# Performance work log

Hardware: AMD Instinct MI355X
Metric: run time of the kernel (lower is better)

The kernel has to match this reference:

```python
import jax, jax.numpy as jnp
import numpy as np

EPS = 1e-5
FH, FW, OC = 1, 9, 32  # filt_h, filt_w, out_channels (hardcoded in HypER)


def _bn(x, g, b, axes):
    # training-mode batchnorm: biased variance over `axes`
    m = jnp.mean(x, axis=axes, keepdims=True)
    v = jnp.mean(jnp.square(x - m), axis=axes, keepdims=True)
    return (x - m) * jax.lax.rsqrt(v + EPS) * g + b


def setup_inputs() -> dict:
    key = jax.random.key(0)
    ks = jax.random.split(key, 8)
    N, INPUT_D, D1, D2, B = 50000, 400, 400, 400, 8192
    fc_len = OC * (D1 - FW + 1)  # 32*392 = 12544
    return {
        "head_tail_id": jax.random.randint(ks[0], (2, B), 0, N, dtype=jnp.int32),
        "unique_entity_embed": jax.random.normal(ks[1], (N, INPUT_D), jnp.float32),
        "W_E": jax.random.normal(ks[2], (INPUT_D, D1), jnp.float32) * 0.05,
        "fc1_w": jax.random.normal(ks[3], (OC * FW, D2), jnp.float32) * 0.05,
        "fc1_b": jnp.zeros((OC * FW,), jnp.float32),
        "fc_w": jax.random.normal(ks[4], (D1, fc_len), jnp.float32) * 0.02,
        "fc_b": jnp.zeros((D1,), jnp.float32),
        "bn0_g": jnp.ones((1,), jnp.float32),
        "bn0_b": jnp.zeros((1,), jnp.float32),
        "bn1_g": jnp.ones((OC,), jnp.float32),
        "bn1_b": jnp.zeros((OC,), jnp.float32),
        "bn2_g": jnp.ones((400,), jnp.float32),
        "bn2_b": jnp.zeros((400,), jnp.float32),
    }


def reference(head_tail_id, unique_entity_embed, W_E, fc1_w, fc1_b, fc_w, fc_b,
              bn0_g, bn0_b, bn1_g, bn1_b, bn2_g, bn2_b):
    E = unique_entity_embed @ W_E                    # (N, d1)
    head = E[head_tail_id[0]]                        # (B, d1)
    tail = E[head_tail_id[1]]                        # (B, d1)
    # bn0: BatchNorm2d with 1 channel -> normalize over all B*1*d1 elements
    x = _bn(head, bn0_g[0], bn0_b[0], axes=(0, 1))   # (B, d1)
    # hypernetwork: per-sample dynamic 1x9 filters for 32 out-channels
    k = (tail @ fc1_w.T + fc1_b).reshape(-1, OC, FW)  # (B, 32, 9)
    W_out = x.shape[1] - FW + 1                       # d1-8 = 392
    win_idx = jnp.arange(W_out)[:, None] + jnp.arange(FW)[None, :]
    xw = x[:, win_idx]                                # (B, W_out, 9) sliding windows
    # grouped conv (groups=B), cross-correlation as in F.conv2d
    conv = jnp.einsum('bjw,bow->boj', xw, k)          # (B, 32, W_out)
    # bn1: per out-channel over (B, W_out)
    conv = _bn(conv, bn1_g[None, :, None], bn1_b[None, :, None], axes=(0, 2))
    feat = conv.reshape(conv.shape[0], -1)            # (B, 32*W_out), channel-major flatten
    out = feat @ fc_w.T + fc_b                        # (B, d1)
    out = _bn(out, bn2_g, bn2_b, axes=(0,))           # BatchNorm1d over batch
    return jax.nn.relu(out)
```

## Files before the change

kernel.cpp:

```cpp
#include <hip/hip_runtime.h>


#define BB   8192
#define DD   400
#define RR   288
#define OCC  32
#define FWW  9
#define JJ   392
#define FCLEN 12544
#define KSPL 4
#define KS   (FCLEN / KSPL)
#define KSTEPS (KS / 64)
#define EPSF 1e-5
#define RB2  512

typedef __attribute__((ext_vector_type(8))) short bf16x8;
typedef __attribute__((ext_vector_type(4))) float f32x4;

__device__ inline unsigned short f2bf(float f) {
    union { float f; unsigned u; } x; x.f = f;
    unsigned r = x.u + 0x7fffu + ((x.u >> 16) & 1u);
    return (unsigned short)(r >> 16);
}

__device__ inline void gload16(const void* g, void* l) {
    __builtin_amdgcn_global_load_lds((const __attribute__((address_space(1))) unsigned int*)g,
                                     (__attribute__((address_space(3))) unsigned int*)l, 16, 0, 0);
}

__device__ inline float block_reduce_256(float v, float* red) {
    #pragma unroll
    for (int m = 1; m < 64; m <<= 1) v += __shfl_xor(v, m);
    int wv = threadIdx.x >> 6;
    if ((threadIdx.x & 63) == 0) red[wv] = v;
    __syncthreads();
    float r = 0.f;
    if (threadIdx.x == 0) r = red[0] + red[1] + red[2] + red[3];
    return r;
}

__global__ __launch_bounds__(256) void prep_M(const float* __restrict__ WE,
                                              const float* __restrict__ f1w,
                                              float* __restrict__ Mout) {
    __shared__ float sA[16][17];
    __shared__ float sB[16][17];
    int tx = threadIdx.x, ty = threadIdx.y;
    int r0 = blockIdx.x * 16, i0 = blockIdx.y * 16;
    float acc = 0.f;
    for (int d0 = 0; d0 < DD; d0 += 16) {
        sA[ty][tx] = WE[(size_t)(i0 + ty) * DD + d0 + tx];
        sB[ty][tx] = f1w[(size_t)(r0 + ty) * DD + d0 + tx];
        __syncthreads();
        #pragma unroll
        for (int dd = 0; dd < 16; ++dd) acc = fmaf(sA[ty][dd], sB[tx][dd], acc);
        __syncthreads();
    }
    Mout[(size_t)(i0 + ty) * RR + r0 + tx] = acc;
}

template <int BN>
__global__ __launch_bounds__(256) void gemm_s1(const float* __restrict__ A,
                                               const int* __restrict__ idx,
                                               const float* __restrict__ Bm,
                                               const float* __restrict__ bias,
                                               float* __restrict__ C, int N,
                                               float* __restrict__ bn0part) {
    constexpr int BNF = BN / 16;
    constexpr int BCH = 64 * (BN / 4) / 256;
    __shared__ unsigned short Al[64][72];
    __shared__ unsigned short Bl[BN][72];
    __shared__ int ridx[64];
    __shared__ float red[8];
    int tid = threadIdx.x;
    int bm = blockIdx.x, bn = blockIdx.y;
    if (tid < 64) ridx[tid] = idx[bm * 64 + tid];
    int lane = tid & 63, wv = tid >> 6;
    int m16 = lane & 15, kb = lane >> 4;
    f32x4 acc[BNF];
    #pragma unroll
    for (int nb = 0; nb < BNF; ++nb) acc[nb] = (f32x4){0.f, 0.f, 0.f, 0.f};
    __syncthreads();

    float4 av[4];
    float4 bv[BCH];
    auto LOADR = [&](int k0) {
        #pragma unroll
        for (int r = 0; r < 4; ++r) {
            int c = tid + 256 * r;
            int row = c >> 4, kq = c & 15;
            int gk = k0 + kq * 4;
            av[r] = (float4){0.f, 0.f, 0.f, 0.f};
            if (gk < DD) av[r] = *(const float4*)(A + (size_t)ridx[row] * DD + gk);
        }
        #pragma unroll
        for (int r = 0; r < BCH; ++r) {
            int c = tid + 256 * r;
            int kk2 = c / (BN / 4), nq = c % (BN / 4);
            int gk = k0 + kk2;
            bv[r] = (float4){0.f, 0.f, 0.f, 0.f};
            if (gk < DD) bv[r] = *(const float4*)(Bm + (size_t)gk * N + bn * BN + nq * 4);
        }
    };
    auto WRITELDS = [&]() {
        #pragma unroll
        for (int r = 0; r < 4; ++r) {
            int c = tid + 256 * r;
            int row = c >> 4, kq = c & 15;
            ushort4 p;
            p.x = f2bf(av[r].x); p.y = f2bf(av[r].y); p.z = f2bf(av[r].z); p.w = f2bf(av[r].w);
            *(ushort4*)&Al[row][kq * 4] = p;
        }
        #pragma unroll
        for (int r = 0; r < BCH; ++r) {
            int c = tid + 256 * r;
            int kk2 = c / (BN / 4), nq = c % (BN / 4);
            Bl[nq * 4 + 0][kk2] = f2bf(bv[r].x);
            Bl[nq * 4 + 1][kk2] = f2bf(bv[r].y);
            Bl[nq * 4 + 2][kk2] = f2bf(bv[r].z);
            Bl[nq * 4 + 3][kk2] = f2bf(bv[r].w);
        }
    };

    LOADR(0);
    for (int kt = 0; kt < 7; ++kt) {
        WRITELDS();
        __syncthreads();
        if (kt + 1 < 7) LOADR((kt + 1) * 64);
        #pragma unroll
        for (int ks = 0; ks < 2; ++ks) {
            bf16x8 a = *(const bf16x8*)&Al[wv * 16 + m16][ks * 32 + kb * 8];
            #pragma unroll
            for (int nb = 0; nb < BNF; ++nb) {
                bf16x8 b = *(const bf16x8*)&Bl[nb * 16 + m16][ks * 32 + kb * 8];
                acc[nb] = __builtin_amdgcn_mfma_f32_16x16x32_bf16(a, b, acc[nb], 0, 0, 0);
            }
        }
        __syncthreads();
    }
    float s1 = 0.f, s2 = 0.f;
    #pragma unroll
    for (int nb = 0; nb < BNF; ++nb)
        #pragma unroll
        for (int rr = 0; rr < 4; ++rr) {
            int gr = bm * 64 + wv * 16 + kb * 4 + rr;
            int gc = bn * BN + nb * 16 + m16;
            float v = acc[nb][rr];
            if (bias) v += bias[gc];
            C[(size_t)gr * N + gc] = v;
            s1 += v; s2 = fmaf(v, v, s2);
        }
    if (bn0part) {
        float t1 = block_reduce_256(s1, red);
        __syncthreads();
        float t2 = block_reduce_256(s2, red);
        if (tid == 0) {
            int pid = bm * gridDim.y + bn;
            bn0part[pid * 2] = t1; bn0part[pid * 2 + 1] = t2;
        }
    }
}

__global__ __launch_bounds__(256) void bn0_fin(const float* __restrict__ part,
                                               const float* __restrict__ g,
                                               const float* __restrict__ b,
                                               float* __restrict__ ab0) {
    __shared__ float red[8];
    float s1 = 0.f, s2 = 0.f;
    for (int i = threadIdx.x; i < 640; i += 256) {
        s1 += part[i * 2]; s2 += part[i * 2 + 1];
    }
    float t1 = block_reduce_256(s1, red);
    __syncthreads();
    float t2 = block_reduce_256(s2, red);
    if (threadIdx.x == 0) {
        double n = (double)BB * DD;
        double mean = (double)t1 / n;
        double var = (double)t2 / n - mean * mean;
        float a0 = (float)((double)g[0] / sqrt(var + EPSF));
        float b0 = (float)((double)b[0] - mean * a0);
        ab0[0] = a0; ab0[1] = b0;
    }
}

__global__ __launch_bounds__(256) void conv_k(const float* __restrict__ head,
                                              const float* __restrict__ kbuf,
                                              const float* __restrict__ ab0,
                                              unsigned short* __restrict__ convb,
                                              float* __restrict__ chpartT) {
    __shared__ float xs[DD];
    __shared__ float ks[RR];
    int b = blockIdx.x, tid = threadIdx.x;
    float a0 = ab0[0], b0 = ab0[1];
    for (int i = tid; i < DD; i += 256) xs[i] = fmaf(head[(size_t)b * DD + i], a0, b0);
    for (int i = tid; i < RR; i += 256) ks[i] = kbuf[(size_t)b * RR + i];
    __syncthreads();
    int lane = tid & 63, wv = tid >> 6;
    unsigned short* orow = convb + (size_t)b * FCLEN;
    float kk[8][FWW];
    #pragma unroll
    for (int oi = 0; oi < 8; ++oi)
        #pragma unroll
        for (int w2 = 0; w2 < FWW; ++w2) kk[oi][w2] = ks[(wv * 8 + oi) * FWW + w2];
    float s1[8], s2[8];
    #pragma unroll
    for (int oi = 0; oi < 8; ++oi) { s1[oi] = 0.f; s2[oi] = 0.f; }
    #pragma unroll
    for (int jt = 0; jt < 2; ++jt) {
        int j0 = jt * 256 + lane * 4;
        if (j0 < JJ) {
            const float4* x4 = (const float4*)xs;
            float4 va = x4[(j0 >> 2)], vb = x4[(j0 >> 2) + 1], vc = x4[(j0 >> 2) + 2];
            float x[12] = {va.x, va.y, va.z, va.w, vb.x, vb.y, vb.z, vb.w, vc.x, vc.y, vc.z, vc.w};
            #pragma unroll
            for (int oi = 0; oi < 8; ++oi) {
                float acc[4];
                #pragma unroll
                for (int q = 0; q < 4; ++q) {
                    float a = 0.f;
                    #pragma unroll
                    for (int w2 = 0; w2 < FWW; ++w2) a = fmaf(x[q + w2], kk[oi][w2], a);
                    acc[q] = a;
                }
                ushort4 p;
                p.x = f2bf(acc[0]); p.y = f2bf(acc[1]); p.z = f2bf(acc[2]); p.w = f2bf(acc[3]);
                *(ushort4*)(orow + (wv * 8 + oi) * JJ + j0) = p;
                #pragma unroll
                for (int q = 0; q < 4; ++q) { s1[oi] += acc[q]; s2[oi] = fmaf(acc[q], acc[q], s2[oi]); }
            }
        }
    }
    #pragma unroll
    for (int oi = 0; oi < 8; ++oi) {
        float a = s1[oi], c = s2[oi];
        #pragma unroll
        for (int m = 1; m < 64; m <<= 1) { a += __shfl_xor(a, m); c += __shfl_xor(c, m); }
        if (lane == 0) {
            int o = wv * 8 + oi;
            chpartT[(size_t)o * BB + b] = a;
            chpartT[(size_t)(OCC + o) * BB + b] = c;
        }
    }
}

__global__ __launch_bounds__(256) void bn1_fin(const float* __restrict__ chpartT,
                                               const float* __restrict__ g1,
                                               const float* __restrict__ b1,
                                               float* __restrict__ alphabeta) {
    __shared__ float red[8];
    int o = blockIdx.x, tid = threadIdx.x;
    float s1 = 0.f, s2 = 0.f;
    for (int t = tid; t < BB; t += 256) {
        s1 += chpartT[(size_t)o * BB + t];
        s2 += chpartT[(size_t)(OCC + o) * BB + t];
    }
    float t1 = block_reduce_256(s1, red);
    __syncthreads();
    float t2 = block_reduce_256(s2, red);
    if (tid == 0) {
        double n = (double)BB * JJ;
        double mean = (double)t1 / n;
        double var = (double)t2 / n - mean * mean;
        float al = (float)((double)g1[o] / sqrt(var + EPSF));
        float be = (float)((double)b1[o] - mean * al);
        alphabeta[o] = al; alphabeta[OCC + o] = be;
    }
}

__global__ __launch_bounds__(256) void prep_fcw(const float* __restrict__ fc_w,
                                                const float* __restrict__ fc_b,
                                                const float* __restrict__ alphabeta,
                                                unsigned short* __restrict__ Bp,
                                                float* __restrict__ bias2) {
    __shared__ float al[OCC], be[OCC];
    __shared__ float red[8];
    int d = blockIdx.x, tid = threadIdx.x;
    if (tid < OCC) { al[tid] = alphabeta[tid]; be[tid] = alphabeta[OCC + tid]; }
    __syncthreads();
    const float* row = fc_w + (size_t)d * FCLEN;
    unsigned short* orow = Bp + (size_t)d * FCLEN;
    float bacc = 0.f;
    for (int o = 0; o < OCC; ++o) {
        float a = al[o], bb = be[o];
        for (int j = tid; j < JJ; j += 256) {
            float wv = row[o * JJ + j];
            orow[o * JJ + j] = f2bf(wv * a);
            bacc = fmaf(wv, bb, bacc);
        }
    }
    float t = block_reduce_256(bacc, red);
    if (tid == 0) bias2[d] = fc_b[d] + t;
}

__global__ __launch_bounds__(256, 3) void fc_gemm_sk(const unsigned short* __restrict__ A,
                                                     const unsigned short* __restrict__ Bp,
                                                     float* __restrict__ P) {
    __shared__ __align__(16) unsigned short Al[256 * 64];
    __shared__ __align__(16) unsigned short Bl[80 * 64];
    int tid = threadIdx.x;
    int orig = blockIdx.x;
    int wgid = (orig & 7) * 80 + (orig >> 3);
    int bn = wgid % 5;
    int rest = wgid / 5;
    int bm = rest & 31;
    int bz = rest >> 5;
    int lane = tid & 63, wv = tid >> 6;
    int m16 = lane & 15, kb = lane >> 4;
    int srow = lane >> 3, scol = lane & 7;
    int sw = m16 & 7;
    f32x4 acc[4][5];
    #pragma unroll
    for (int mi = 0; mi < 4; ++mi)
        #pragma unroll
        for (int nb = 0; nb < 5; ++nb) acc[mi][nb] = (f32x4){0.f, 0.f, 0.f, 0.f};

    const unsigned short* Asrc = A + (size_t)(bm * 256 + srow) * FCLEN
                                   + (size_t)bz * KS + ((scol ^ srow) << 3);
    const unsigned short* Bsrc = Bp + (size_t)(bn * 80 + srow) * FCLEN
                                   + (size_t)bz * KS + ((scol ^ srow) << 3);

    for (int kt = 0; kt < KSTEPS; ++kt) {
        const size_t koff = (size_t)kt * 64;
        #pragma unroll
        for (int i = 0; i < 11; ++i) {
            int c = wv + i * 4;
            if (c < 32) {
                gload16(Asrc + (size_t)c * 8 * FCLEN + koff, Al + c * 512);
            } else if (c < 42) {
                int cb = c - 32;
                gload16(Bsrc + (size_t)cb * 8 * FCLEN + koff, Bl + cb * 512);
            }
        }
        __syncthreads();
        #pragma unroll
        for (int ks2 = 0; ks2 < 2; ++ks2) {
            int ch = (((ks2 * 4 + kb) ^ sw) << 3);
            bf16x8 a[4];
            #pragma unroll
            for (int mi = 0; mi < 4; ++mi)
                a[mi] = *(const bf16x8*)(Al + (wv * 64 + mi * 16 + m16) * 64 + ch);
            #pragma unroll
            for (int nb = 0; nb < 5; ++nb) {
                bf16x8 b = *(const bf16x8*)(Bl + (nb * 16 + m16) * 64 + ch);
                #pragma unroll
                for (int mi = 0; mi < 4; ++mi)
                    acc[mi][nb] = __builtin_amdgcn_mfma_f32_16x16x32_bf16(a[mi], b, acc[mi][nb], 0, 0, 0);
            }
        }
        __syncthreads();
    }

    float* Po = P + (size_t)bz * BB * DD;
    #pragma unroll
    for (int mi = 0; mi < 4; ++mi)
        #pragma unroll
        for (int nb = 0; nb < 5; ++nb)
            #pragma unroll
            for (int rr = 0; rr < 4; ++rr) {
                int gr = bm * 256 + wv * 64 + mi * 16 + kb * 4 + rr;
                int gc = bn * 80 + nb * 16 + m16;
                Po[(size_t)gr * DD + gc] = acc[mi][nb][rr];
            }
}

__global__ __launch_bounds__(256) void reduce_bn2(const float* __restrict__ P,
                                                  const float* __restrict__ bias2,
                                                  float* __restrict__ out,
                                                  float* __restrict__ part) {
    int blk = blockIdx.x, tid = threadIdx.x;
    int r0 = blk * 16;
    const size_t S = (size_t)BB * DD;
    bool hasb = tid < DD - 256;
    float bia = bias2[tid];
    float bib = hasb ? bias2[256 + tid] : 0.f;
    float s1a = 0.f, s2a = 0.f, s1b = 0.f, s2b = 0.f;
    for (int r = 0; r < 16; ++r) {
        size_t base = (size_t)(r0 + r) * DD;
        float v = P[base + tid] + P[S + base + tid] + P[2 * S + base + tid] + P[3 * S + base + tid] + bia;
        out[base + tid] = v;
        s1a += v; s2a = fmaf(v, v, s2a);
        if (hasb) {
            size_t b2i = base + 256 + tid;
            float u = P[b2i] + P[S + b2i] + P[2 * S + b2i] + P[3 * S + b2i] + bib;
            out[b2i] = u;
            s1b += u; s2b = fmaf(u, u, s2b);
        }
    }
    float* p = part + (size_t)blk * (DD * 2);
    p[tid * 2] = s1a; p[tid * 2 + 1] = s2a;
    if (hasb) { p[(256 + tid) * 2] = s1b; p[(256 + tid) * 2 + 1] = s2b; }
}

__global__ __launch_bounds__(128) void bn2_fin(const float* __restrict__ part,
                                               const float* __restrict__ g2,
                                               const float* __restrict__ b2,
                                               float* __restrict__ sc,
                                               float* __restrict__ sh) {
    __shared__ float red[4];
    int col = blockIdx.x, tid = threadIdx.x;
    float s1 = 0.f, s2 = 0.f;
    for (int t = tid; t < RB2; t += 128) {
        s1 += part[(size_t)t * (DD * 2) + col * 2];
        s2 += part[(size_t)t * (DD * 2) + col * 2 + 1];
    }
    #pragma unroll
    for (int m = 1; m < 64; m <<= 1) { s1 += __shfl_xor(s1, m); s2 += __shfl_xor(s2, m); }
    int wv = tid >> 6;
    if ((tid & 63) == 0) { red[wv] = s1; red[2 + wv] = s2; }
    __syncthreads();
    if (tid == 0) {
        double t1 = (double)red[0] + red[1];
        double t2 = (double)red[2] + red[3];
        double mean = t1 / (double)BB;
        double var = t2 / (double)BB - mean * mean;
        float s = (float)((double)g2[col] / sqrt(var + EPSF));
        sc[col] = s;
        sh[col] = (float)((double)b2[col] - mean * s);
    }
}

__global__ __launch_bounds__(256) void final_k(float* __restrict__ out,
                                               const float* __restrict__ sc,
                                               const float* __restrict__ sh) {
    __shared__ float lsc[DD], lsh[DD];
    int tid = threadIdx.x;
    for (int c = tid; c < DD; c += 256) { lsc[c] = sc[c]; lsh[c] = sh[c]; }
    __syncthreads();
    size_t base = (size_t)blockIdx.x * 4 * DD;
    for (int r = 0; r < 4; ++r)
        for (int c = tid; c < DD; c += 256) {
            size_t i = base + (size_t)r * DD + c;
            float v = fmaf(out[i], lsc[c], lsh[c]);
            out[i] = v > 0.f ? v : 0.f;
        }
}

extern "C" void kernel_launch(void* const* d_in, const int* in_sizes, int n_in,
                              void* d_out, int out_size, void* d_ws, size_t ws_size,
                              hipStream_t stream) {
    const int* ht      = (const int*)d_in[0];
    const float* UE    = (const float*)d_in[1];
    const float* W_E   = (const float*)d_in[2];
    const float* fc1_w = (const float*)d_in[3];
    const float* fc1_b = (const float*)d_in[4];
    const float* fc_w  = (const float*)d_in[5];
    const float* fc_b  = (const float*)d_in[6];
    const float* bn0_g = (const float*)d_in[7];
    const float* bn0_b = (const float*)d_in[8];
    const float* bn1_g = (const float*)d_in[9];
    const float* bn1_b = (const float*)d_in[10];
    const float* bn2_g = (const float*)d_in[11];
    const float* bn2_b = (const float*)d_in[12];
    float* out = (float*)d_out;

    char* w = (char*)d_ws;
    unsigned short* convb = (unsigned short*)w; w += (size_t)BB * FCLEN * 2;
    unsigned short* Bprep = (unsigned short*)w; w += (size_t)DD * FCLEN * 2;
    float* chpartT = (float*)w; w += (size_t)2 * OCC * BB * 4;
    float* bn0p = (float*)w;  w += 640 * 2 * 4;
    float* ab0 = (float*)w;   w += 64;
    float* alphabeta = (float*)w; w += 64 * 4;
    float* bias2 = (float*)w; w += DD * 4;
    float* bn2p = (float*)w;  w += (size_t)RB2 * DD * 2 * 4;
    float* bn2sc = (float*)w; w += DD * 4;
    float* bn2sh = (float*)w; w += DD * 4;
    float* P = (float*)w;     w += (size_t)KSPL * BB * DD * 4;
    float* head = P;
    float* kbuf = head + (size_t)BB * DD;
    float* Mbuf = kbuf + (size_t)BB * RR;
    (void)ws_size; (void)in_sizes; (void)n_in; (void)out_size;

    prep_M<<<dim3(RR / 16, DD / 16), dim3(16, 16), 0, stream>>>(W_E, fc1_w, Mbuf);
    gemm_s1<80><<<dim3(BB / 64, DD / 80), 256, 0, stream>>>(UE, ht, W_E, nullptr, head, DD, bn0p);
    gemm_s1<96><<<dim3(BB / 64, RR / 96), 256, 0, stream>>>(UE, ht + BB, Mbuf, fc1_b, kbuf, RR, nullptr);
    bn0_fin<<<1, 256, 0, stream>>>(bn0p, bn0_g, bn0_b, ab0);
    conv_k<<<BB, 256, 0, stream>>>(head, kbuf, ab0, convb, chpartT);
    bn1_fin<<<OCC, 256, 0, stream>>>(chpartT, bn1_g, bn1_b, alphabeta);
    prep_fcw<<<DD, 256, 0, stream>>>(fc_w, fc_b, alphabeta, Bprep, bias2);
    fc_gemm_sk<<<dim3(32 * 5 * KSPL), 256, 0, stream>>>(convb, Bprep, P);
    reduce_bn2<<<RB2, 256, 0, stream>>>(P, bias2, out, bn2p);
    bn2_fin<<<DD, 128, 0, stream>>>(bn2p, bn2_g, bn2_b, bn2sc, bn2sh);
    final_k<<<2048, 256, 0, stream>>>(out, bn2sc, bn2sh);
}
```

Baseline: 336.1 us.

## Double-buffer LDS tiles in split-K FC GEMM with async prefetch

Reworks the split-K FC GEMM main loop to use two LDS buffers with a K-step of 32 instead of a single buffer with a K-step of 64. The next tile's global-to-LDS loads are issued before the current tile's MFMAs, and explicit vmcnt waits plus raw barriers replace the two __syncthreads per iteration. The intent is to overlap global memory latency with MFMA work; it also raises wave priority around the MFMA block. The trade-off is twice as many iterations and barriers, hand-counted vmcnt values that must match each wave's load count, and a changed swizzle pattern.

```diff
diff --git a/kernel.cpp b/kernel.cpp
--- a/kernel.cpp
+++ b/kernel.cpp
@@ -10,7 +10,7 @@
 #define FCLEN 12544
 #define KSPL 4
 #define KS   (FCLEN / KSPL)
-#define KSTEPS (KS / 64)
+#define KST32 (KS / 32)
 #define EPSF 1e-5
 #define RB2  512
 
@@ -294,8 +294,8 @@
 __global__ __launch_bounds__(256, 3) void fc_gemm_sk(const unsigned short* __restrict__ A,
                                                      const unsigned short* __restrict__ Bp,
                                                      float* __restrict__ P) {
-    __shared__ __align__(16) unsigned short Al[256 * 64];
-    __shared__ __align__(16) unsigned short Bl[80 * 64];
+    __shared__ __align__(16) unsigned short Al[2][256 * 32];
+    __shared__ __align__(16) unsigned short Bl[2][80 * 32];
     int tid = threadIdx.x;
     int orig = blockIdx.x;
     int wgid = (orig & 7) * 80 + (orig >> 3);
@@ -305,8 +305,8 @@
     int bz = rest >> 5;
     int lane = tid & 63, wv = tid >> 6;
     int m16 = lane & 15, kb = lane >> 4;
-    int srow = lane >> 3, scol = lane & 7;
-    int sw = m16 & 7;
+    int srow = lane >> 2, scol = lane & 3;
+    int sw = m16 & 3;
     f32x4 acc[4][5];
     #pragma unroll
     for (int mi = 0; mi < 4; ++mi)
@@ -314,39 +314,55 @@
         for (int nb = 0; nb < 5; ++nb) acc[mi][nb] = (f32x4){0.f, 0.f, 0.f, 0.f};
 
     const unsigned short* Asrc = A + (size_t)(bm * 256 + srow) * FCLEN
-                                   + (size_t)bz * KS + ((scol ^ srow) << 3);
+                                   + (size_t)bz * KS + ((scol ^ (srow & 3)) << 3);
     const unsigned short* Bsrc = Bp + (size_t)(bn * 80 + srow) * FCLEN
-                                   + (size_t)bz * KS + ((scol ^ srow) << 3);
-
-    for (int kt = 0; kt < KSTEPS; ++kt) {
-        const size_t koff = (size_t)kt * 64;
-        #pragma unroll
-        for (int i = 0; i < 11; ++i) {
+                                   + (size_t)bz * KS + ((scol ^ (srow & 3)) << 3);
+
+    auto STAGE = [&](int t, int buf) {
+        const size_t koff = (size_t)t * 32;
+        #pragma unroll
+        for (int i = 0; i < 6; ++i) {
             int c = wv + i * 4;
-            if (c < 32) {
-                gload16(Asrc + (size_t)c * 8 * FCLEN + koff, Al + c * 512);
-            } else if (c < 42) {
-                int cb = c - 32;
-                gload16(Bsrc + (size_t)cb * 8 * FCLEN + koff, Bl + cb * 512);
+            if (c < 16) {
+                gload16(Asrc + (size_t)c * 16 * FCLEN + koff, &Al[buf][c * 512]);
+            } else if (c < 21) {
+                int cb = c - 16;
+                gload16(Bsrc + (size_t)cb * 16 * FCLEN + koff, &Bl[buf][cb * 512]);
             }
         }
-        __syncthreads();
-        #pragma unroll
-        for (int ks2 = 0; ks2 < 2; ++ks2) {
-            int ch = (((ks2 * 4 + kb) ^ sw) << 3);
-            bf16x8 a[4];
+    };
+
+    STAGE(0, 0);
+    for (int t = 0; t < KST32; ++t) {
+        if (t + 1 < KST32) {
+            STAGE(t + 1, (t + 1) & 1);
+            if (wv == 0) asm volatile("s_waitcnt vmcnt(6)" ::: "memory");
+            else         asm volatile("s_waitcnt vmcnt(5)" ::: "memory");
+        } else {
+            asm volatile("s_waitcnt vmcnt(0)" ::: "memory");
+        }
+        __builtin_amdgcn_s_barrier();
+        __builtin_amdgcn_sched_barrier(0);
+        const unsigned short* Ac = &Al[t & 1][0];
+        const unsigned short* Bc = &Bl[t & 1][0];
+        int ch = ((kb ^ sw) << 3);
+        bf16x8 a[4];
+        #pragma unroll
+        for (int mi = 0; mi < 4; ++mi)
+            a[mi] = *(const bf16x8*)(Ac + (wv * 64 + mi * 16 + m16) * 32 + ch);
+        __builtin_amdgcn_s_setprio(1);
+        #pragma unroll
+        for (int nb = 0; nb < 5; ++nb) {
+            bf16x8 b = *(const bf16x8*)(Bc + (nb * 16 + m16) * 32 + ch);
             #pragma unroll
             for (int mi = 0; mi < 4; ++mi)
-                a[mi] = *(const bf16x8*)(Al + (wv * 64 + mi * 16 + m16) * 64 + ch);
-            #pragma unroll
-            for (int nb = 0; nb < 5; ++nb) {
-                bf16x8 b = *(const bf16x8*)(Bl + (nb * 16 + m16) * 64 + ch);
-                #pragma unroll
-                for (int mi = 0; mi < 4; ++mi)
-                    acc[mi][nb] = __builtin_amdgcn_mfma_f32_16x16x32_bf16(a[mi], b, acc[mi][nb], 0, 0, 0);
-            }
-        }
-        __syncthreads();
+                acc[mi][nb] = __builtin_amdgcn_mfma_f32_16x16x32_bf16(a[mi], b, acc[mi][nb], 0, 0, 0);
+        }
+        __builtin_amdgcn_s_setprio(0);
+        asm volatile("s_waitcnt lgkmcnt(0)" ::: "memory");
+        __builtin_amdgcn_sched_barrier(0);
+        __builtin_amdgcn_s_barrier();
+        __builtin_amdgcn_sched_barrier(0);
     }
 
     float* Po = P + (size_t)bz * BB * DD;
```

After: 348.9 us. 3.8% more time.
